# Kernel tuning notes

Measured on AMD Instinct MI355X. Metric: run time of the kernel, lower is better.

The kernel has to match this reference:

```python
import jax, jax.numpy as jnp
import numpy as np

ALPHA = 0.0  # module init alpha
BETA = 1.0   # default beta in set_target_with_data


def setup_inputs() -> dict:
    key = jax.random.key(0)
    k1, k2, k3, k4 = jax.random.split(key, 4)
    B, H, KP, N, D = 4, 16, 512, 4096, 64
    return {
        "K": jax.random.normal(k1, (B, H, KP, D), dtype=jnp.float32),
        "V": jax.random.normal(k2, (B, H, KP, D), dtype=jnp.float32),
        "xk": jax.random.normal(k3, (B, H, N, D), dtype=jnp.float32),
        "xv": jax.random.normal(k4, (B, H, N, D), dtype=jnp.float32),
    }


def reference(K, V, xk, xv):
    # set_target_with_data with dist_metric='dot', beta=1.0, beta2=None
    # dists: (B, H, k, n) = K @ xk^T
    dists = jnp.einsum('bhkd,bhnd->bhkn', K, xk)
    # softmax over the memory-slot axis (dim=-2)
    dk = jax.nn.softmax(BETA * dists, axis=-2)
    # normalize over the data axis (dim=-1)
    dkx = dk / jnp.sum(dk, axis=-1, keepdims=True)
    # weighted readout of data queries/values
    K_target = jnp.einsum('bhkn,bhnd->bhkd', dkx, xk)
    V_target = jnp.einsum('bhkn,bhnd->bhkd', dkx, xv)
    # set_target: grads used by maximize-SGD update
    gK = (1.0 - ALPHA) * (K_target - K)
    gV = (1.0 - ALPHA) * (V_target - V)
    return jnp.stack((gK, gV), axis=0)  # (2, B, H, k, d)
```

## Files before the change

kernel.cpp:

```cpp
#include <hip/hip_runtime.h>
#include <hip/hip_bf16.h>

typedef __bf16 bf16_t;
typedef __attribute__((ext_vector_type(8))) __bf16 bf16x8;
typedef __attribute__((ext_vector_type(4))) float f32x4;
typedef __attribute__((ext_vector_type(16))) float f32x16;

#define BH 64
#define KP 512
#define NN 4096
#define DD 64
#define GSZ (BH * KP * DD)

#define MFMA16(a, b, c) __builtin_amdgcn_mfma_f32_16x16x32_bf16((a), (b), (c), 0, 0, 0)
#define MFMA32(a, b, c) __builtin_amdgcn_mfma_f32_32x32x16_bf16((a), (b), (c), 0, 0, 0)

__device__ __forceinline__ bf16x8 cvt8v(const f32x4 lo, const f32x4 hi) {
  bf16x8 r;
  r[0] = (bf16_t)lo[0]; r[1] = (bf16_t)lo[1]; r[2] = (bf16_t)lo[2]; r[3] = (bf16_t)lo[3];
  r[4] = (bf16_t)hi[0]; r[5] = (bf16_t)hi[1]; r[6] = (bf16_t)hi[2]; r[7] = (bf16_t)hi[3];
  return r;
}
__device__ __forceinline__ bf16x8 cvt8(const float* __restrict__ p) {
  return cvt8v(*(const f32x4*)p, *(const f32x4*)(p + 4));
}
__device__ __forceinline__ unsigned pack2(float a, float b) {
  union { bf16_t h[2]; unsigned u; } x;
  x.h[0] = (bf16_t)a; x.h[1] = (bf16_t)b;
  return x.u;
}

__device__ __forceinline__ void stage16(bf16_t* lds_base, const bf16_t* gsrc) {
  __builtin_amdgcn_global_load_lds(
      (const __attribute__((address_space(1))) void*)gsrc,
      (__attribute__((address_space(3))) void*)lds_base, 16, 0, 0);
}

__global__ __launch_bounds__(256) void hop_prep(
    const float* __restrict__ xk, const float* __restrict__ xv,
    bf16_t* __restrict__ xk16, bf16_t* __restrict__ xkT16, bf16_t* __restrict__ xvT16)
{
  __shared__ __align__(16) bf16_t T[64 * 72];
  const int t = threadIdx.x;
  const int n0 = blockIdx.x * 64;
  const int bh = blockIdx.y;
  const int row = t >> 2;
  const int d0  = (t & 3) * 16;
  const int dcol = t >> 2;
  const int nb   = (t & 3) * 16;
  const size_t gb  = (size_t)bh * NN * DD;
  const size_t gbT = (size_t)bh * DD * NN;

  {
    const float* src = xk + gb + (size_t)(n0 + row) * DD + d0;
    const f32x4 a0 = *(const f32x4*)(src);
    const f32x4 a1 = *(const f32x4*)(src + 4);
    const f32x4 a2 = *(const f32x4*)(src + 8);
    const f32x4 a3 = *(const f32x4*)(src + 12);
    const bf16x8 lo = cvt8v(a0, a1), hi = cvt8v(a2, a3);
    bf16_t* dn = xk16 + gb + (size_t)(n0 + row) * DD + d0;
    *(bf16x8*)(dn)     = lo;
    *(bf16x8*)(dn + 8) = hi;
    *(bf16x8*)(T + row * 72 + d0)     = lo;
    *(bf16x8*)(T + row * 72 + d0 + 8) = hi;
  }
  __syncthreads();
  {
    bf16x8 o0, o1;
    #pragma unroll
    for (int j = 0; j < 8; j++) o0[j] = T[(nb + j) * 72 + dcol];
    #pragma unroll
    for (int j = 0; j < 8; j++) o1[j] = T[(nb + 8 + j) * 72 + dcol];
    bf16_t* dT = xkT16 + gbT + (size_t)dcol * NN + n0 + nb;
    *(bf16x8*)(dT)     = o0;
    *(bf16x8*)(dT + 8) = o1;
  }
  __syncthreads();
  {
    const float* src = xv + gb + (size_t)(n0 + row) * DD + d0;
    const f32x4 a0 = *(const f32x4*)(src);
    const f32x4 a1 = *(const f32x4*)(src + 4);
    const f32x4 a2 = *(const f32x4*)(src + 8);
    const f32x4 a3 = *(const f32x4*)(src + 12);
    *(bf16x8*)(T + row * 72 + d0)     = cvt8v(a0, a1);
    *(bf16x8*)(T + row * 72 + d0 + 8) = cvt8v(a2, a3);
  }
  __syncthreads();
  {
    bf16x8 o0, o1;
    #pragma unroll
    for (int j = 0; j < 8; j++) o0[j] = T[(nb + j) * 72 + dcol];
    #pragma unroll
    for (int j = 0; j < 8; j++) o1[j] = T[(nb + 8 + j) * 72 + dcol];
    bf16_t* dT = xvT16 + gbT + (size_t)dcol * NN + n0 + nb;
    *(bf16x8*)(dT)     = o0;
    *(bf16x8*)(dT + 8) = o1;
  }
}

__global__ __launch_bounds__(256) void hop_pass1(
    const float* __restrict__ Km, const bf16_t* __restrict__ xk16,
    float* __restrict__ inv_colsum)
{
  __shared__ __align__(16) bf16_t Ks[128 * 72];

  const int tid  = threadIdx.x;
  const int wave = tid >> 6, lane = tid & 63;
  const int col  = lane & 15, quad = lane >> 4;
  const int bid  = blockIdx.x;
  const int bh   = (bid & 7) + 8 * ((bid >> 3) & 7);
  const int n0   = (bid >> 6) * 256 + wave * 64;

  const float*  Kb   = Km   + (size_t)bh * KP * DD;
  const bf16_t* xkb  = xk16 + (size_t)bh * NN * DD;

  bf16x8 bf[4][2];
  #pragma unroll
  for (int nsub = 0; nsub < 4; nsub++) {
    const bf16_t* p = xkb + (size_t)(n0 + nsub * 16 + col) * DD + quad * 8;
    bf[nsub][0] = *(const bf16x8*)(p);
    bf[nsub][1] = *(const bf16x8*)(p + 32);
  }

  float colacc[4] = {0.f, 0.f, 0.f, 0.f};
  const int srow = tid >> 1, sdo = (tid & 1) * 32;

  for (int kc = 0; kc < KP; kc += 128) {
    __syncthreads();
    const float* src = Kb + (size_t)(kc + srow) * DD + sdo;
    #pragma unroll
    for (int u = 0; u < 4; u++) {
      const f32x4 p0 = *(const f32x4*)(src + 8 * u);
      const f32x4 p1 = *(const f32x4*)(src + 8 * u + 4);
      *(bf16x8*)(Ks + srow * 72 + sdo + 8 * u) = cvt8v(p0, p1);
    }
    __syncthreads();
    #pragma unroll
    for (int ks = 0; ks < 8; ks++) {
      const bf16x8 a0 = *(const bf16x8*)(Ks + (ks * 16 + col) * 72 + quad * 8);
      const bf16x8 a1 = *(const bf16x8*)(Ks + (ks * 16 + col) * 72 + 32 + quad * 8);
      #pragma unroll
      for (int nsub = 0; nsub < 4; nsub++) {
        f32x4 c = {0.f, 0.f, 0.f, 0.f};
        c = MFMA16(a0, bf[nsub][0], c);
        c = MFMA16(a1, bf[nsub][1], c);
        colacc[nsub] += __expf(c[0]) + __expf(c[1]) + __expf(c[2]) + __expf(c[3]);
      }
    }
  }
  #pragma unroll
  for (int nsub = 0; nsub < 4; nsub++) {
    colacc[nsub] += __shfl_xor(colacc[nsub], 16, 64);
    colacc[nsub] += __shfl_xor(colacc[nsub], 32, 64);
  }
  float v = colacc[0];
  v = (quad == 1) ? colacc[1] : v;
  v = (quad == 2) ? colacc[2] : v;
  v = (quad == 3) ? colacc[3] : v;
  inv_colsum[bh * NN + n0 + quad * 16 + col] = 1.0f / v;
}

#define NT 64

__global__ __launch_bounds__(256) void hop_pass2(
    const float* __restrict__ Km, const float* __restrict__ Vm,
    const bf16_t* __restrict__ xk16, const bf16_t* __restrict__ xkT16,
    const bf16_t* __restrict__ xvT16,
    const float* __restrict__ inv_colsum, float* __restrict__ out)
{
  __shared__ __align__(16) bf16_t xks[2][NT * DD];
  __shared__ __align__(16) bf16_t xkT[2][DD * NT];
  __shared__ __align__(16) bf16_t xvT[2][DD * NT];
  __shared__ float rows_lds[4][32];

  const int tid  = threadIdx.x;
  const int wave = tid >> 6, lane = tid & 63;
  const int col  = lane & 31, hi = lane >> 5;
  const int bid  = blockIdx.x;
  const int m    = bid >> 3;
  const int bh   = (bid & 7) + 8 * (m >> 2);
  const int kblk = m & 3;
  const int k0w  = kblk * 128 + wave * 32;

  const float*  Kb   = Km    + (size_t)bh * KP * DD;
  const float*  Vb   = Vm    + (size_t)bh * KP * DD;
  const bf16_t* xkb  = xk16  + (size_t)bh * NN * DD;
  const bf16_t* xkTb = xkT16 + (size_t)bh * DD * NN;
  const bf16_t* xvTb = xvT16 + (size_t)bh * DD * NN;
  const float*  inv  = inv_colsum + bh * NN;

  bf16x8 bk[4];
  #pragma unroll
  for (int t = 0; t < 4; t++)
    bk[t] = cvt8(Kb + (size_t)(k0w + col) * DD + t * 16 + hi * 8);

  f32x16 accK[2], accV[2];
  #pragma unroll
  for (int i = 0; i < 2; i++) {
    #pragma unroll
    for (int r = 0; r < 16; r++) { accK[i][r] = 0.f; accV[i][r] = 0.f; }
  }
  float rowacc = 0.f;

  const int srl = lane >> 3;
  const int r0  = wave * 16 + srl;
  const int r1  = r0 + 8;
  const int sb  = ((lane & 7) ^ srl) * 8;
  const int lb0 = (wave * 2 + 0) * 512;
  const int lb1 = (wave * 2 + 1) * 512;

  stage16(&xks[0][lb0], xkb + (size_t)r0 * DD + sb);
  stage16(&xks[0][lb1], xkb + (size_t)r1 * DD + sb);
  stage16(&xkT[0][lb0], xkTb + (size_t)r0 * NN + sb);
  stage16(&xkT[0][lb1], xkTb + (size_t)r1 * NN + sb);
  stage16(&xvT[0][lb0], xvTb + (size_t)r0 * NN + sb);
  stage16(&xvT[0][lb1], xvTb + (size_t)r1 * NN + sb);
  __syncthreads();

  int cur = 0;
  for (int n0 = 0; n0 < NN; n0 += NT) {
    if (n0 + NT < NN) {
      const int nx = n0 + NT;
      const int nb2 = cur ^ 1;
      stage16(&xks[nb2][lb0], xkb + (size_t)(nx + r0) * DD + sb);
      stage16(&xks[nb2][lb1], xkb + (size_t)(nx + r1) * DD + sb);
      stage16(&xkT[nb2][lb0], xkTb + (size_t)r0 * NN + nx + sb);
      stage16(&xkT[nb2][lb1], xkTb + (size_t)r1 * NN + nx + sb);
      stage16(&xvT[nb2][lb0], xvTb + (size_t)r0 * NN + nx + sb);
      stage16(&xvT[nb2][lb1], xvTb + (size_t)r1 * NN + nx + sb);
    }

    const bf16_t* xs = xks[cur];
    bf16x8 wa[4];

    #pragma unroll
    for (int nh = 0; nh < 2; nh++) {
      f32x4 icv[4];
      #pragma unroll
      for (int q = 0; q < 4; q++)
        icv[q] = *(const f32x4*)(inv + n0 + 32 * nh + 8 * q + 4 * hi);

      const int n  = nh * 32 + col;
      const int rb = n * DD;
      f32x16 s;
      #pragma unroll
      for (int r = 0; r < 16; r++) s[r] = 0.f;
      #pragma unroll
      for (int t = 0; t < 4; t++) {
        const bf16x8 a = *(const bf16x8*)(xs + rb + (((2 * t + hi) ^ (n & 7)) << 3));
        s = MFMA32(a, bk[t], s);
      }
      #pragma unroll
      for (int b = 0; b < 2; b++) {
        float p[8];
        #pragma unroll
        for (int j = 0; j < 8; j++)
          p[j] = __expf(s[8 * b + j]) * icv[2 * b + (j >> 2)][j & 3];
        rowacc += ((p[0] + p[1]) + (p[2] + p[3])) + ((p[4] + p[5]) + (p[6] + p[7]));
        unsigned q0a = pack2(p[0], p[1]), q0b = pack2(p[2], p[3]);
        unsigned q1a = pack2(p[4], p[5]), q1b = pack2(p[6], p[7]);
        asm("v_permlane32_swap_b32 %0, %1" : "+v"(q0a), "+v"(q1a));
        asm("v_permlane32_swap_b32 %0, %1" : "+v"(q0b), "+v"(q1b));
        union { unsigned u[4]; bf16x8 v; } f;
        f.u[0] = q0a; f.u[1] = q0b; f.u[2] = q1a; f.u[3] = q1b;
        wa[nh * 2 + b] = f.v;
      }
    }

    #pragma unroll
    for (int dg = 0; dg < 2; dg++) {
      const int d   = dg * 32 + col;
      const int rbd = d * NT;
      const bf16_t* kp = xkT[cur];
      const bf16_t* vp = xvT[cur];
      #pragma unroll
      for (int c = 0; c < 4; c++) {
        const int off = rbd + (((2 * c + hi) ^ (d & 7)) << 3);
        const bf16x8 bkf = *(const bf16x8*)(kp + off);
        const bf16x8 bvf = *(const bf16x8*)(vp + off);
        accK[dg] = MFMA32(wa[c], bkf, accK[dg]);
        accV[dg] = MFMA32(wa[c], bvf, accV[dg]);
      }
    }

    __syncthreads();
    cur ^= 1;
  }

  rowacc += __shfl_xor(rowacc, 32, 64);
  rows_lds[wave][col] = 1.0f / rowacc;

  const size_t base = (size_t)bh * KP * DD;
  #pragma unroll
  for (int dg = 0; dg < 2; dg++) {
    #pragma unroll
    for (int r = 0; r < 16; r++) {
      const int kw = (r & 3) + 8 * (r >> 2) + 4 * hi;
      const float invr = rows_lds[wave][kw];
      const int k = k0w + kw;
      const int d = dg * 32 + col;
      const size_t idx = base + (size_t)k * DD + d;
      out[idx]       = accK[dg][r] * invr - Kb[(size_t)k * DD + d];
      out[GSZ + idx] = accV[dg][r] * invr - Vb[(size_t)k * DD + d];
    }
  }
}

#define PW 72

__global__ __launch_bounds__(256) void hop_pass1_fb(
    const float* __restrict__ Km, const float* __restrict__ xk,
    float* __restrict__ inv_colsum)
{
  __shared__ __align__(16) bf16_t Ks[128 * 72];
  const int tid  = threadIdx.x;
  const int wave = tid >> 6, lane = tid & 63;
  const int col  = lane & 15, quad = lane >> 4;
  const int bh = blockIdx.y;
  const int n0 = blockIdx.x * 256 + wave * 64;
  const float* Kb  = Km + (size_t)bh * KP * DD;
  const float* xkb = xk + (size_t)bh * NN * DD;
  bf16x8 bf[4][2];
  #pragma unroll
  for (int nsub = 0; nsub < 4; nsub++) {
    const float* p = xkb + (size_t)(n0 + nsub * 16 + col) * DD + quad * 8;
    bf[nsub][0] = cvt8(p);
    bf[nsub][1] = cvt8(p + 32);
  }
  float colacc[4] = {0.f, 0.f, 0.f, 0.f};
  const int srow = tid >> 1, sdo = (tid & 1) * 32;
  for (int kc = 0; kc < KP; kc += 128) {
    __syncthreads();
    const float* src = Kb + (size_t)(kc + srow) * DD + sdo;
    #pragma unroll
    for (int u = 0; u < 4; u++) {
      const f32x4 p0 = *(const f32x4*)(src + 8 * u);
      const f32x4 p1 = *(const f32x4*)(src + 8 * u + 4);
      *(bf16x8*)(Ks + srow * 72 + sdo + 8 * u) = cvt8v(p0, p1);
    }
    __syncthreads();
    #pragma unroll
    for (int ks = 0; ks < 8; ks++) {
      const bf16x8 a0 = *(const bf16x8*)(Ks + (ks * 16 + col) * 72 + quad * 8);
      const bf16x8 a1 = *(const bf16x8*)(Ks + (ks * 16 + col) * 72 + 32 + quad * 8);
      #pragma unroll
      for (int nsub = 0; nsub < 4; nsub++) {
        f32x4 c = {0.f, 0.f, 0.f, 0.f};
        c = MFMA16(a0, bf[nsub][0], c);
        c = MFMA16(a1, bf[nsub][1], c);
        colacc[nsub] += __expf(c[0]) + __expf(c[1]) + __expf(c[2]) + __expf(c[3]);
      }
    }
  }
  #pragma unroll
  for (int nsub = 0; nsub < 4; nsub++) {
    colacc[nsub] += __shfl_xor(colacc[nsub], 16, 64);
    colacc[nsub] += __shfl_xor(colacc[nsub], 32, 64);
  }
  float v = colacc[0];
  v = (quad == 1) ? colacc[1] : v;
  v = (quad == 2) ? colacc[2] : v;
  v = (quad == 3) ? colacc[3] : v;
  inv_colsum[bh * NN + n0 + quad * 16 + col] = 1.0f / v;
}

__global__ __launch_bounds__(256) void hop_pass2_fb(
    const float* __restrict__ Km, const float* __restrict__ Vm,
    const float* __restrict__ xk, const float* __restrict__ xv,
    const float* __restrict__ inv_colsum, float* __restrict__ out)
{
  __shared__ __align__(16) bf16_t xksf[NT * PW];
  __shared__ __align__(16) bf16_t xkTf[DD * NT];
  __shared__ __align__(16) bf16_t xvTf[DD * NT];
  __shared__ __align__(16) bf16_t wtf[4][16 * PW];

  const int tid  = threadIdx.x;
  const int wave = tid >> 6, lane = tid & 63;
  const int col  = lane & 15, quad = lane >> 4;
  const int bh   = blockIdx.x >> 3;
  const int k0   = (blockIdx.x & 7) * 64 + wave * 16;

  const float* Kb  = Km + (size_t)bh * KP * DD;
  const float* Vb  = Vm + (size_t)bh * KP * DD;
  const float* xkb = xk + (size_t)bh * NN * DD;
  const float* xvb = xv + (size_t)bh * NN * DD;
  const float* inv = inv_colsum + bh * NN;

  const bf16x8 ak0 = cvt8(Kb + (size_t)(k0 + col) * DD + quad * 8);
  const bf16x8 ak1 = cvt8(Kb + (size_t)(k0 + col) * DD + 32 + quad * 8);

  f32x4 accK[4], accV[4];
  #pragma unroll
  for (int i = 0; i < 4; i++) {
    accK[i] = (f32x4){0.f, 0.f, 0.f, 0.f};
    accV[i] = (f32x4){0.f, 0.f, 0.f, 0.f};
  }
  float rows_part = 0.f;

  const int sn = tid >> 2;
  const int sd = (tid & 3) * 16;
  const int shi = sn >> 3, slo = sn & 7;

  for (int n0 = 0; n0 < NN; n0 += NT) {
    f32x4 gk[4], gv[4];
    #pragma unroll
    for (int u = 0; u < 4; u++) {
      gk[u] = *(const f32x4*)(xkb + (size_t)(n0 + sn) * DD + sd + 4 * u);
      gv[u] = *(const f32x4*)(xvb + (size_t)(n0 + sn) * DD + sd + 4 * u);
    }
    float ic[4];
    #pragma unroll
    for (int nsub = 0; nsub < 4; nsub++) ic[nsub] = inv[n0 + nsub * 16 + col];

    __syncthreads();
    *(bf16x8*)(xksf + sn * PW + sd)     = cvt8v(gk[0], gk[1]);
    *(bf16x8*)(xksf + sn * PW + sd + 8) = cvt8v(gk[2], gk[3]);
    #pragma unroll
    for (int j = 0; j < 16; j++) {
      const int d   = sd + j;
      const int off = d * NT + (((shi) ^ (d >> 3)) << 3) + slo;
      xkTf[off] = (bf16_t)gk[j >> 2][j & 3];
      xvTf[off] = (bf16_t)gv[j >> 2][j & 3];
    }
    __syncthreads();

    f32x4 s[4];
    #pragma unroll
    for (int nsub = 0; nsub < 4; nsub++) {
      const bf16x8 b0 = *(const bf16x8*)(xksf + (nsub * 16 + col) * PW + quad * 8);
      const bf16x8 b1 = *(const bf16x8*)(xksf + (nsub * 16 + col) * PW + 32 + quad * 8);
      f32x4 c = {0.f, 0.f, 0.f, 0.f};
      c = MFMA16(ak0, b0, c);
      c = MFMA16(ak1, b1, c);
      s[nsub] = c;
    }
    bf16_t* wr = wtf[wave];
    #pragma unroll
    for (int nsub = 0; nsub < 4; nsub++) {
      #pragma unroll
      for (int r = 0; r < 4; r++)
        wr[(quad * 4 + r) * PW + nsub * 16 + col] = (bf16_t)(__expf(s[nsub][r]) * ic[nsub]);
    }
    const bf16x8 wa0 = *(const bf16x8*)(wr + col * PW + quad * 8);
    const bf16x8 wa1 = *(const bf16x8*)(wr + col * PW + 32 + quad * 8);
    #pragma unroll
    for (int j = 0; j < 8; j++) rows_part += (float)wa0[j] + (float)wa1[j];

    #pragma unroll
    for (int dt = 0; dt < 4; dt++) {
      const int d = dt * 16 + col, dhi = d >> 3;
      const bf16x8 bk0 = *(const bf16x8*)(xkTf + d * NT + ((quad ^ dhi) << 3));
      const bf16x8 bk1 = *(const bf16x8*)(xkTf + d * NT + (((4 + quad) ^ dhi) << 3));
      const bf16x8 bv0 = *(const bf16x8*)(xvTf + d * NT + ((quad ^ dhi) << 3));
      const bf16x8 bv1 = *(const bf16x8*)(xvTf + d * NT + (((4 + quad) ^ dhi) << 3));
      accK[dt] = MFMA16(wa0, bk0, accK[dt]);
      accK[dt] = MFMA16(wa1, bk1, accK[dt]);
      accV[dt] = MFMA16(wa0, bv0, accV[dt]);
      accV[dt] = MFMA16(wa1, bv1, accV[dt]);
    }
  }

  float rs = rows_part;
  rs += __shfl_xor(rs, 16, 64);
  rs += __shfl_xor(rs, 32, 64);
  float invrs[4];
  #pragma unroll
  for (int r = 0; r < 4; r++) invrs[r] = 1.0f / __shfl(rs, quad * 4 + r, 64);

  const size_t base = (size_t)bh * KP * DD;
  #pragma unroll
  for (int dt = 0; dt < 4; dt++) {
    #pragma unroll
    for (int r = 0; r < 4; r++) {
      const int k = k0 + quad * 4 + r;
      const int d = dt * 16 + col;
      const size_t idx = base + (size_t)k * DD + d;
      out[idx]       = accK[dt][r] * invrs[r] - Kb[(size_t)k * DD + d];
      out[GSZ + idx] = accV[dt][r] * invrs[r] - Vb[(size_t)k * DD + d];
    }
  }
}

extern "C" void kernel_launch(void* const* d_in, const int* in_sizes, int n_in,
                              void* d_out, int out_size, void* d_ws, size_t ws_size,
                              hipStream_t stream)
{
  (void)in_sizes; (void)n_in; (void)out_size;
  const float* Km = (const float*)d_in[0];
  const float* Vm = (const float*)d_in[1];
  const float* xk = (const float*)d_in[2];
  const float* xv = (const float*)d_in[3];
  float* out = (float*)d_out;
  float* inv_colsum = (float*)d_ws;

  const size_t SCRE = (size_t)BH * NN * DD;
  const size_t NEED = (size_t)BH * NN * sizeof(float) + 3 * SCRE * sizeof(bf16_t);

  if (ws_size >= NEED) {
    bf16_t* xk16  = (bf16_t*)((char*)d_ws + (size_t)BH * NN * sizeof(float));
    bf16_t* xkT16 = xk16 + SCRE;
    bf16_t* xvT16 = xkT16 + SCRE;
    hop_prep<<<dim3(NN / 64, BH), 256, 0, stream>>>(xk, xv, xk16, xkT16, xvT16);
    hop_pass1<<<dim3((NN / 256) * BH), 256, 0, stream>>>(Km, xk16, inv_colsum);
    hop_pass2<<<dim3(BH * 4), 256, 0, stream>>>(Km, Vm, xk16, xkT16, xvT16,
                                                inv_colsum, out);
  } else {
    hop_pass1_fb<<<dim3(NN / 256, BH), 256, 0, stream>>>(Km, xk, inv_colsum);
    hop_pass2_fb<<<dim3(BH * (KP / 64)), 256, 0, stream>>>(Km, Vm, xk, xv,
                                                           inv_colsum, out);
  }
}
```

Before: 329.7 us.

## Split pass2 over the data axis into two halves with a reduction kernel

Splits the second pass along the N (data) dimension into two halves, so twice as many blocks (512 instead of 256) can fill the GPU. Each half writes partial K/V accumulators and partial row sums to workspace, and a new elementwise kernel combines them, normalises and subtracts K/V. A second fallback path with a 16x16 MFMA variant of pass2 is also added for a smaller workspace. The cost is an extra kernel launch plus extra global traffic for the partial results, and the path depends on the workspace being large enough.

```diff
diff --git a/kernel.cpp b/kernel.cpp
--- a/kernel.cpp
+++ b/kernel.cpp
@@ -11,6 +11,8 @@
 #define NN 4096
 #define DD 64
 #define GSZ (BH * KP * DD)
+#define NT 64
+#define NHALF 2048
 
 #define MFMA16(a, b, c) __builtin_amdgcn_mfma_f32_16x16x32_bf16((a), (b), (c), 0, 0, 0)
 #define MFMA32(a, b, c) __builtin_amdgcn_mfma_f32_32x32x16_bf16((a), (b), (c), 0, 0, 0)
@@ -160,30 +162,29 @@
   inv_colsum[bh * NN + n0 + quad * 16 + col] = 1.0f / v;
 }
 
-#define NT 64
-
-__global__ __launch_bounds__(256) void hop_pass2(
-    const float* __restrict__ Km, const float* __restrict__ Vm,
+__global__ __launch_bounds__(256) void hop_pass2s(
+    const float* __restrict__ Km,
     const bf16_t* __restrict__ xk16, const bf16_t* __restrict__ xkT16,
     const bf16_t* __restrict__ xvT16,
-    const float* __restrict__ inv_colsum, float* __restrict__ out)
+    const float* __restrict__ inv_colsum,
+    float* __restrict__ pK, float* __restrict__ pV, float* __restrict__ prs)
 {
   __shared__ __align__(16) bf16_t xks[2][NT * DD];
   __shared__ __align__(16) bf16_t xkT[2][DD * NT];
   __shared__ __align__(16) bf16_t xvT[2][DD * NT];
-  __shared__ float rows_lds[4][32];
 
   const int tid  = threadIdx.x;
   const int wave = tid >> 6, lane = tid & 63;
   const int col  = lane & 31, hi = lane >> 5;
   const int bid  = blockIdx.x;
-  const int m    = bid >> 3;
-  const int bh   = (bid & 7) + 8 * (m >> 2);
-  const int kblk = m & 3;
+  const int bh   = (bid & 7) + 8 * ((bid >> 3) & 7);
+  const int sub  = bid >> 6;
+  const int kblk = sub & 3;
+  const int nh   = sub >> 2;
   const int k0w  = kblk * 128 + wave * 32;
+  const int nbase = nh * NHALF;
 
   const float*  Kb   = Km    + (size_t)bh * KP * DD;
-  const float*  Vb   = Vm    + (size_t)bh * KP * DD;
   const bf16_t* xkb  = xk16  + (size_t)bh * NN * DD;
   const bf16_t* xkTb = xkT16 + (size_t)bh * DD * NN;
   const bf16_t* xvTb = xvT16 + (size_t)bh * DD * NN;
@@ -209,17 +210,17 @@
   const int lb0 = (wave * 2 + 0) * 512;
   const int lb1 = (wave * 2 + 1) * 512;
 
-  stage16(&xks[0][lb0], xkb + (size_t)r0 * DD + sb);
-  stage16(&xks[0][lb1], xkb + (size_t)r1 * DD + sb);
-  stage16(&xkT[0][lb0], xkTb + (size_t)r0 * NN + sb);
-  stage16(&xkT[0][lb1], xkTb + (size_t)r1 * NN + sb);
-  stage16(&xvT[0][lb0], xvTb + (size_t)r0 * NN + sb);
-  stage16(&xvT[0][lb1], xvTb + (size_t)r1 * NN + sb);
+  stage16(&xks[0][lb0], xkb + (size_t)(nbase + r0) * DD + sb);
+  stage16(&xks[0][lb1], xkb + (size_t)(nbase + r1) * DD + sb);
+  stage16(&xkT[0][lb0], xkTb + (size_t)r0 * NN + nbase + sb);
+  stage16(&xkT[0][lb1], xkTb + (size_t)r1 * NN + nbase + sb);
+  stage16(&xvT[0][lb0], xvTb + (size_t)r0 * NN + nbase + sb);
+  stage16(&xvT[0][lb1], xvTb + (size_t)r1 * NN + nbase + sb);
   __syncthreads();
 
   int cur = 0;
-  for (int n0 = 0; n0 < NN; n0 += NT) {
-    if (n0 + NT < NN) {
+  for (int n0 = nbase; n0 < nbase + NHALF; n0 += NT) {
+    if (n0 + NT < nbase + NHALF) {
       const int nx = n0 + NT;
       const int nb2 = cur ^ 1;
       stage16(&xks[nb2][lb0], xkb + (size_t)(nx + r0) * DD + sb);
@@ -234,13 +235,13 @@
     bf16x8 wa[4];
 
     #pragma unroll
-    for (int nh = 0; nh < 2; nh++) {
+    for (int g = 0; g < 2; g++) {
       f32x4 icv[4];
       #pragma unroll
       for (int q = 0; q < 4; q++)
-        icv[q] = *(const f32x4*)(inv + n0 + 32 * nh + 8 * q + 4 * hi);
-
-      const int n  = nh * 32 + col;
+        icv[q] = *(const f32x4*)(inv + n0 + 32 * g + 8 * q + 4 * hi);
+
+      const int n  = g * 32 + col;
       const int rb = n * DD;
       f32x16 s;
       #pragma unroll
@@ -263,7 +264,7 @@
         asm("v_permlane32_swap_b32 %0, %1" : "+v"(q0b), "+v"(q1b));
         union { unsigned u[4]; bf16x8 v; } f;
         f.u[0] = q0a; f.u[1] = q0b; f.u[2] = q1a; f.u[3] = q1b;
-        wa[nh * 2 + b] = f.v;
+        wa[g * 2 + b] = f.v;
       }
     }
 
@@ -288,20 +289,189 @@
   }
 
   rowacc += __shfl_xor(rowacc, 32, 64);
-  rows_lds[wave][col] = 1.0f / rowacc;
-
-  const size_t base = (size_t)bh * KP * DD;
+  if (hi == 0) prs[((size_t)nh * BH + bh) * KP + k0w + col] = rowacc;
+
+  float* pKb = pK + ((size_t)(nh * BH + bh) * KP) * DD;
+  float* pVb = pV + ((size_t)(nh * BH + bh) * KP) * DD;
   #pragma unroll
   for (int dg = 0; dg < 2; dg++) {
     #pragma unroll
     for (int r = 0; r < 16; r++) {
       const int kw = (r & 3) + 8 * (r >> 2) + 4 * hi;
-      const float invr = rows_lds[wave][kw];
       const int k = k0w + kw;
       const int d = dg * 32 + col;
+      pKb[(size_t)k * DD + d] = accK[dg][r];
+      pVb[(size_t)k * DD + d] = accV[dg][r];
+    }
+  }
+}
+
+__global__ __launch_bounds__(256) void hop_fin(
+    const float* __restrict__ Km, const float* __restrict__ Vm,
+    const float* __restrict__ pK, const float* __restrict__ pV,
+    const float* __restrict__ prs, float* __restrict__ out)
+{
+  const int t = blockIdx.x * 256 + threadIdx.x;
+  const size_t e  = (size_t)t * 8;
+  const size_t kk = e >> 6;
+  const size_t off = e;
+  const size_t plane = (size_t)BH * KP * DD;
+
+  const float invr = 1.0f / (prs[kk] + prs[(size_t)BH * KP + kk]);
+
+  const f32x4 ka0 = *(const f32x4*)(pK + off);
+  const f32x4 ka1 = *(const f32x4*)(pK + off + 4);
+  const f32x4 kb0 = *(const f32x4*)(pK + plane + off);
+  const f32x4 kb1 = *(const f32x4*)(pK + plane + off + 4);
+  const f32x4 va0 = *(const f32x4*)(pV + off);
+  const f32x4 va1 = *(const f32x4*)(pV + off + 4);
+  const f32x4 vb0 = *(const f32x4*)(pV + plane + off);
+  const f32x4 vb1 = *(const f32x4*)(pV + plane + off + 4);
+  const f32x4 K0  = *(const f32x4*)(Km + off);
+  const f32x4 K1  = *(const f32x4*)(Km + off + 4);
+  const f32x4 V0  = *(const f32x4*)(Vm + off);
+  const f32x4 V1  = *(const f32x4*)(Vm + off + 4);
+
+  f32x4 rk0 = (ka0 + kb0) * invr - K0;
+  f32x4 rk1 = (ka1 + kb1) * invr - K1;
+  f32x4 rv0 = (va0 + vb0) * invr - V0;
+  f32x4 rv1 = (va1 + vb1) * invr - V1;
+
+  *(f32x4*)(out + off)            = rk0;
+  *(f32x4*)(out + off + 4)        = rk1;
+  *(f32x4*)(out + GSZ + off)      = rv0;
+  *(f32x4*)(out + GSZ + off + 4)  = rv1;
+}
+
+__global__ __launch_bounds__(256) void hop_pass2m(
+    const float* __restrict__ Km, const float* __restrict__ Vm,
+    const bf16_t* __restrict__ xk16, const bf16_t* __restrict__ xkT16,
+    const bf16_t* __restrict__ xvT16,
+    const float* __restrict__ inv_colsum, float* __restrict__ out)
+{
+  __shared__ __align__(16) bf16_t xks[2][NT * DD];
+  __shared__ __align__(16) bf16_t xkT[2][DD * NT];
+  __shared__ __align__(16) bf16_t xvT[2][DD * NT];
+  __shared__ __align__(16) bf16_t wt[4][16 * 72];
+
+  const int tid  = threadIdx.x;
+  const int wave = tid >> 6, lane = tid & 63;
+  const int col  = lane & 15, quad = lane >> 4;
+  const int bid  = blockIdx.x;
+  const int bh   = (bid & 7) + 8 * ((bid >> 3) & 7);
+  const int k0   = (bid >> 6) * 64 + wave * 16;
+
+  const float*  Kb   = Km    + (size_t)bh * KP * DD;
+  const float*  Vb   = Vm    + (size_t)bh * KP * DD;
+  const bf16_t* xkb  = xk16  + (size_t)bh * NN * DD;
+  const bf16_t* xkTb = xkT16 + (size_t)bh * DD * NN;
+  const bf16_t* xvTb = xvT16 + (size_t)bh * DD * NN;
+  const float*  inv  = inv_colsum + bh * NN;
+
+  const bf16x8 ak0 = cvt8(Kb + (size_t)(k0 + col) * DD + quad * 8);
+  const bf16x8 ak1 = cvt8(Kb + (size_t)(k0 + col) * DD + 32 + quad * 8);
+
+  f32x4 accK[4], accV[4];
+  #pragma unroll
+  for (int i = 0; i < 4; i++) {
+    accK[i] = (f32x4){0.f, 0.f, 0.f, 0.f};
+    accV[i] = (f32x4){0.f, 0.f, 0.f, 0.f};
+  }
+  float rows_part = 0.f;
+
+  const int srl = lane >> 3;
+  const int r0  = wave * 16 + srl;
+  const int r1  = r0 + 8;
+  const int sb  = ((lane & 7) ^ srl) * 8;
+  const int lb0 = (wave * 2 + 0) * 512;
+  const int lb1 = (wave * 2 + 1) * 512;
+
+  stage16(&xks[0][lb0], xkb + (size_t)r0 * DD + sb);
+  stage16(&xks[0][lb1], xkb + (size_t)r1 * DD + sb);
+  stage16(&xkT[0][lb0], xkTb + (size_t)r0 * NN + sb);
+  stage16(&xkT[0][lb1], xkTb + (size_t)r1 * NN + sb);
+  stage16(&xvT[0][lb0], xvTb + (size_t)r0 * NN + sb);
+  stage16(&xvT[0][lb1], xvTb + (size_t)r1 * NN + sb);
+  __syncthreads();
+
+  int cur = 0;
+  for (int n0 = 0; n0 < NN; n0 += NT) {
+    if (n0 + NT < NN) {
+      const int nx = n0 + NT;
+      const int nb2 = cur ^ 1;
+      stage16(&xks[nb2][lb0], xkb + (size_t)(nx + r0) * DD + sb);
+      stage16(&xks[nb2][lb1], xkb + (size_t)(nx + r1) * DD + sb);
+      stage16(&xkT[nb2][lb0], xkTb + (size_t)r0 * NN + nx + sb);
+      stage16(&xkT[nb2][lb1], xkTb + (size_t)r1 * NN + nx + sb);
+      stage16(&xvT[nb2][lb0], xvTb + (size_t)r0 * NN + nx + sb);
+      stage16(&xvT[nb2][lb1], xvTb + (size_t)r1 * NN + nx + sb);
+    }
+
+    float ic[4];
+    #pragma unroll
+    for (int ns = 0; ns < 4; ns++) ic[ns] = inv[n0 + ns * 16 + col];
+
+    const int key = col & 7;
+
+    f32x4 s[4];
+    #pragma unroll
+    for (int ns = 0; ns < 4; ns++) {
+      const bf16_t* bp = &xks[cur][(ns * 16 + col) * DD];
+      const bf16x8 b0 = *(const bf16x8*)(bp + 8 * (quad ^ key));
+      const bf16x8 b1 = *(const bf16x8*)(bp + 8 * ((quad + 4) ^ key));
+      f32x4 c = {0.f, 0.f, 0.f, 0.f};
+      c = MFMA16(ak0, b0, c);
+      c = MFMA16(ak1, b1, c);
+      s[ns] = c;
+    }
+    bf16_t* wr = wt[wave];
+    #pragma unroll
+    for (int ns = 0; ns < 4; ns++) {
+      #pragma unroll
+      for (int r = 0; r < 4; r++)
+        wr[(quad * 4 + r) * 72 + ns * 16 + col] = (bf16_t)(__expf(s[ns][r]) * ic[ns]);
+    }
+    const bf16x8 wa0 = *(const bf16x8*)(wr + col * 72 + quad * 8);
+    const bf16x8 wa1 = *(const bf16x8*)(wr + col * 72 + 32 + quad * 8);
+    #pragma unroll
+    for (int j = 0; j < 8; j++) rows_part += (float)wa0[j] + (float)wa1[j];
+
+    #pragma unroll
+    for (int dt = 0; dt < 4; dt++) {
+      const int d = dt * 16 + col;
+      const bf16_t* kp = &xkT[cur][d * NT];
+      const bf16_t* vp = &xvT[cur][d * NT];
+      const bf16x8 bk0 = *(const bf16x8*)(kp + 8 * (quad ^ key));
+      const bf16x8 bk1 = *(const bf16x8*)(kp + 8 * ((quad + 4) ^ key));
+      const bf16x8 bv0 = *(const bf16x8*)(vp + 8 * (quad ^ key));
+      const bf16x8 bv1 = *(const bf16x8*)(vp + 8 * ((quad + 4) ^ key));
+      accK[dt] = MFMA16(wa0, bk0, accK[dt]);
+      accK[dt] = MFMA16(wa1, bk1, accK[dt]);
+      accV[dt] = MFMA16(wa0, bv0, accV[dt]);
+      accV[dt] = MFMA16(wa1, bv1, accV[dt]);
+    }
+
+    __syncthreads();
+    cur ^= 1;
+  }
+
+  float rs = rows_part;
+  rs += __shfl_xor(rs, 16, 64);
+  rs += __shfl_xor(rs, 32, 64);
+  float invrs[4];
+  #pragma unroll
+  for (int r = 0; r < 4; r++) invrs[r] = 1.0f / __shfl(rs, quad * 4 + r, 64);
+
+  const size_t base = (size_t)bh * KP * DD;
+  #pragma unroll
+  for (int dt = 0; dt < 4; dt++) {
+    #pragma unroll
+    for (int r = 0; r < 4; r++) {
+      const int k = k0 + quad * 4 + r;
+      const int d = dt * 16 + col;
       const size_t idx = base + (size_t)k * DD + d;
-      out[idx]       = accK[dg][r] * invr - Kb[(size_t)k * DD + d];
-      out[GSZ + idx] = accV[dg][r] * invr - Vb[(size_t)k * DD + d];
+      out[idx]       = accK[dt][r] * invrs[r] - Kb[(size_t)k * DD + d];
+      out[GSZ + idx] = accV[dt][r] * invrs[r] - Vb[(size_t)k * DD + d];
     }
   }
 }
@@ -491,19 +661,36 @@
   const float* xk = (const float*)d_in[2];
   const float* xv = (const float*)d_in[3];
   float* out = (float*)d_out;
+
+  const size_t INVB = (size_t)BH * NN * sizeof(float);
+  const size_t SCRE = (size_t)BH * NN * DD;
+  const size_t NEED  = INVB + 3 * SCRE * sizeof(bf16_t);
+  const size_t PPART = (size_t)2 * BH * KP * DD;
+  const size_t NEED2 = NEED + (2 * PPART + (size_t)2 * BH * KP) * sizeof(float);
+
   float* inv_colsum = (float*)d_ws;
 
-  const size_t SCRE = (size_t)BH * NN * DD;
-  const size_t NEED = (size_t)BH * NN * sizeof(float) + 3 * SCRE * sizeof(bf16_t);
-
-  if (ws_size >= NEED) {
-    bf16_t* xk16  = (bf16_t*)((char*)d_ws + (size_t)BH * NN * sizeof(float));
+  if (ws_size >= NEED2) {
+    bf16_t* xk16  = (bf16_t*)((char*)d_ws + INVB);
+    bf16_t* xkT16 = xk16 + SCRE;
+    bf16_t* xvT16 = xkT16 + SCRE;
+    float*  pK    = (float*)(xvT16 + SCRE);
+    float*  pV    = pK + PPART;
+    float*  prs   = pV + PPART;
+    hop_prep<<<dim3(NN / 64, BH), 256, 0, stream>>>(xk, xv, xk16, xkT16, xvT16);
+    hop_pass1<<<dim3((NN / 256) * BH), 256, 0, stream>>>(Km, xk16, inv_colsum);
+    hop_pass2s<<<dim3(512), 256, 0, stream>>>(Km, xk16, xkT16, xvT16,
+                                              inv_colsum, pK, pV, prs);
+    hop_fin<<<dim3((BH * KP * DD) / (256 * 8)), 256, 0, stream>>>(Km, Vm, pK, pV,
+                                                                  prs, out);
+  } else if (ws_size >= NEED) {
+    bf16_t* xk16  = (bf16_t*)((char*)d_ws + INVB);
     bf16_t* xkT16 = xk16 + SCRE;
     bf16_t* xvT16 = xkT16 + SCRE;
     hop_prep<<<dim3(NN / 64, BH), 256, 0, stream>>>(xk, xv, xk16, xkT16, xvT16);
     hop_pass1<<<dim3((NN / 256) * BH), 256, 0, stream>>>(Km, xk16, inv_colsum);
-    hop_pass2<<<dim3(BH * 4), 256, 0, stream>>>(Km, Vm, xk16, xkT16, xvT16,
-                                                inv_colsum, out);
+    hop_pass2m<<<dim3(BH * (KP / 64)), 256, 0, stream>>>(Km, Vm, xk16, xkT16, xvT16,
+                                                         inv_colsum, out);
   } else {
     hop_pass1_fb<<<dim3(NN / 256, BH), 256, 0, stream>>>(Km, xk, inv_colsum);
     hop_pass2_fb<<<dim3(BH * (KP / 64)), 256, 0, stream>>>(Km, Vm, xk, xv,
```

New measurement: 303.3 us. 1.09x faster.

## Fuse prep into pass1 and split pass2 over N with reduction kernel

Applied to the files above, without the earlier changes.

Merges the bf16 conversion and transpose prep kernel into the column-sum pass, so each block converts its own xk/xv tiles and takes MFMA operands straight from LDS. Pass2 is split along the data axis into NS segments, raising the grid from 256 to 1024 blocks to fill more CUs. Per-segment partial K/V sums and row sums go to workspace, and a new finalize kernel reduces them, normalizes and subtracts K/V. This adds a kernel launch and extra partial-sum memory traffic in exchange for better occupancy of pass2.

```diff
diff --git a/kernel.cpp b/kernel.cpp
--- a/kernel.cpp
+++ b/kernel.cpp
@@ -11,6 +11,7 @@
 #define NN 4096
 #define DD 64
 #define GSZ (BH * KP * DD)
+#define NT 64
 
 #define MFMA16(a, b, c) __builtin_amdgcn_mfma_f32_16x16x32_bf16((a), (b), (c), 0, 0, 0)
 #define MFMA32(a, b, c) __builtin_amdgcn_mfma_f32_32x32x16_bf16((a), (b), (c), 0, 0, 0)
@@ -36,90 +37,89 @@
       (__attribute__((address_space(3))) void*)lds_base, 16, 0, 0);
 }
 
-__global__ __launch_bounds__(256) void hop_prep(
-    const float* __restrict__ xk, const float* __restrict__ xv,
-    bf16_t* __restrict__ xk16, bf16_t* __restrict__ xkT16, bf16_t* __restrict__ xvT16)
-{
-  __shared__ __align__(16) bf16_t T[64 * 72];
-  const int t = threadIdx.x;
-  const int n0 = blockIdx.x * 64;
-  const int bh = blockIdx.y;
-  const int row = t >> 2;
-  const int d0  = (t & 3) * 16;
-  const int dcol = t >> 2;
-  const int nb   = (t & 3) * 16;
-  const size_t gb  = (size_t)bh * NN * DD;
-  const size_t gbT = (size_t)bh * DD * NN;
-
-  {
-    const float* src = xk + gb + (size_t)(n0 + row) * DD + d0;
-    const f32x4 a0 = *(const f32x4*)(src);
-    const f32x4 a1 = *(const f32x4*)(src + 4);
-    const f32x4 a2 = *(const f32x4*)(src + 8);
-    const f32x4 a3 = *(const f32x4*)(src + 12);
-    const bf16x8 lo = cvt8v(a0, a1), hi = cvt8v(a2, a3);
-    bf16_t* dn = xk16 + gb + (size_t)(n0 + row) * DD + d0;
-    *(bf16x8*)(dn)     = lo;
-    *(bf16x8*)(dn + 8) = hi;
-    *(bf16x8*)(T + row * 72 + d0)     = lo;
-    *(bf16x8*)(T + row * 72 + d0 + 8) = hi;
-  }
-  __syncthreads();
-  {
-    bf16x8 o0, o1;
-    #pragma unroll
-    for (int j = 0; j < 8; j++) o0[j] = T[(nb + j) * 72 + dcol];
-    #pragma unroll
-    for (int j = 0; j < 8; j++) o1[j] = T[(nb + 8 + j) * 72 + dcol];
-    bf16_t* dT = xkT16 + gbT + (size_t)dcol * NN + n0 + nb;
-    *(bf16x8*)(dT)     = o0;
-    *(bf16x8*)(dT + 8) = o1;
-  }
-  __syncthreads();
-  {
-    const float* src = xv + gb + (size_t)(n0 + row) * DD + d0;
-    const f32x4 a0 = *(const f32x4*)(src);
-    const f32x4 a1 = *(const f32x4*)(src + 4);
-    const f32x4 a2 = *(const f32x4*)(src + 8);
-    const f32x4 a3 = *(const f32x4*)(src + 12);
-    *(bf16x8*)(T + row * 72 + d0)     = cvt8v(a0, a1);
-    *(bf16x8*)(T + row * 72 + d0 + 8) = cvt8v(a2, a3);
-  }
-  __syncthreads();
-  {
-    bf16x8 o0, o1;
-    #pragma unroll
-    for (int j = 0; j < 8; j++) o0[j] = T[(nb + j) * 72 + dcol];
-    #pragma unroll
-    for (int j = 0; j < 8; j++) o1[j] = T[(nb + 8 + j) * 72 + dcol];
-    bf16_t* dT = xvT16 + gbT + (size_t)dcol * NN + n0 + nb;
-    *(bf16x8*)(dT)     = o0;
-    *(bf16x8*)(dT + 8) = o1;
-  }
-}
-
-__global__ __launch_bounds__(256) void hop_pass1(
-    const float* __restrict__ Km, const bf16_t* __restrict__ xk16,
-    float* __restrict__ inv_colsum)
+__global__ __launch_bounds__(256) void hop_p1f(
+    const float* __restrict__ Km, const float* __restrict__ xk,
+    const float* __restrict__ xv,
+    bf16_t* __restrict__ xk16, bf16_t* __restrict__ xkT16,
+    bf16_t* __restrict__ xvT16, float* __restrict__ inv_colsum)
 {
   __shared__ __align__(16) bf16_t Ks[128 * 72];
+  bf16_t* T = Ks;
 
   const int tid  = threadIdx.x;
   const int wave = tid >> 6, lane = tid & 63;
   const int col  = lane & 15, quad = lane >> 4;
   const int bid  = blockIdx.x;
   const int bh   = (bid & 7) + 8 * ((bid >> 3) & 7);
-  const int n0   = (bid >> 6) * 256 + wave * 64;
-
-  const float*  Kb   = Km   + (size_t)bh * KP * DD;
-  const bf16_t* xkb  = xk16 + (size_t)bh * NN * DD;
+  const int nblk = (bid >> 6) * 256;
+
+  const float* Kb  = Km + (size_t)bh * KP * DD;
+  const size_t gb  = (size_t)bh * NN * DD;
+  const size_t gbT = (size_t)bh * DD * NN;
+
+  const int row  = tid >> 2;
+  const int d0   = (tid & 3) * 16;
+  const int dcol = tid >> 2;
+  const int nb   = (tid & 3) * 16;
 
   bf16x8 bf[4][2];
-  #pragma unroll
-  for (int nsub = 0; nsub < 4; nsub++) {
-    const bf16_t* p = xkb + (size_t)(n0 + nsub * 16 + col) * DD + quad * 8;
-    bf[nsub][0] = *(const bf16x8*)(p);
-    bf[nsub][1] = *(const bf16x8*)(p + 32);
+
+  #pragma unroll
+  for (int b = 0; b < 4; b++) {
+    const int nbase = nblk + b * 64;
+    {
+      const float* src = xk + gb + (size_t)(nbase + row) * DD + d0;
+      const f32x4 a0 = *(const f32x4*)(src);
+      const f32x4 a1 = *(const f32x4*)(src + 4);
+      const f32x4 a2 = *(const f32x4*)(src + 8);
+      const f32x4 a3 = *(const f32x4*)(src + 12);
+      const bf16x8 lo = cvt8v(a0, a1), hi = cvt8v(a2, a3);
+      bf16_t* dn = xk16 + gb + (size_t)(nbase + row) * DD + d0;
+      *(bf16x8*)(dn)     = lo;
+      *(bf16x8*)(dn + 8) = hi;
+      *(bf16x8*)(T + row * 72 + d0)     = lo;
+      *(bf16x8*)(T + row * 72 + d0 + 8) = hi;
+    }
+    __syncthreads();
+    {
+      bf16x8 o0, o1;
+      #pragma unroll
+      for (int j = 0; j < 8; j++) o0[j] = T[(nb + j) * 72 + dcol];
+      #pragma unroll
+      for (int j = 0; j < 8; j++) o1[j] = T[(nb + 8 + j) * 72 + dcol];
+      bf16_t* dT = xkT16 + gbT + (size_t)dcol * NN + nbase + nb;
+      *(bf16x8*)(dT)     = o0;
+      *(bf16x8*)(dT + 8) = o1;
+      if (wave == b) {
+        #pragma unroll
+        for (int nsub = 0; nsub < 4; nsub++) {
+          bf[nsub][0] = *(const bf16x8*)(T + (nsub * 16 + col) * 72 + quad * 8);
+          bf[nsub][1] = *(const bf16x8*)(T + (nsub * 16 + col) * 72 + 32 + quad * 8);
+        }
+      }
+    }
+    __syncthreads();
+    {
+      const float* src = xv + gb + (size_t)(nbase + row) * DD + d0;
+      const f32x4 a0 = *(const f32x4*)(src);
+      const f32x4 a1 = *(const f32x4*)(src + 4);
+      const f32x4 a2 = *(const f32x4*)(src + 8);
+      const f32x4 a3 = *(const f32x4*)(src + 12);
+      *(bf16x8*)(T + row * 72 + d0)     = cvt8v(a0, a1);
+      *(bf16x8*)(T + row * 72 + d0 + 8) = cvt8v(a2, a3);
+    }
+    __syncthreads();
+    {
+      bf16x8 o0, o1;
+      #pragma unroll
+      for (int j = 0; j < 8; j++) o0[j] = T[(nb + j) * 72 + dcol];
+      #pragma unroll
+      for (int j = 0; j < 8; j++) o1[j] = T[(nb + 8 + j) * 72 + dcol];
+      bf16_t* dT = xvT16 + gbT + (size_t)dcol * NN + nbase + nb;
+      *(bf16x8*)(dT)     = o0;
+      *(bf16x8*)(dT + 8) = o1;
+    }
+    __syncthreads();
   }
 
   float colacc[4] = {0.f, 0.f, 0.f, 0.f};
@@ -157,33 +157,35 @@
   v = (quad == 1) ? colacc[1] : v;
   v = (quad == 2) ? colacc[2] : v;
   v = (quad == 3) ? colacc[3] : v;
-  inv_colsum[bh * NN + n0 + quad * 16 + col] = 1.0f / v;
-}
-
-#define NT 64
-
-__global__ __launch_bounds__(256) void hop_pass2(
-    const float* __restrict__ Km, const float* __restrict__ Vm,
+  inv_colsum[bh * NN + nblk + wave * 64 + quad * 16 + col] = 1.0f / v;
+}
+
+template <int NS>
+__global__ __launch_bounds__(256) void hop_pass2s(
+    const float* __restrict__ Km,
     const bf16_t* __restrict__ xk16, const bf16_t* __restrict__ xkT16,
     const bf16_t* __restrict__ xvT16,
-    const float* __restrict__ inv_colsum, float* __restrict__ out)
+    const float* __restrict__ inv_colsum,
+    float* __restrict__ pK, float* __restrict__ pV, float* __restrict__ prs)
 {
+  constexpr int NSEG = NN / NS;
+
   __shared__ __align__(16) bf16_t xks[2][NT * DD];
   __shared__ __align__(16) bf16_t xkT[2][DD * NT];
   __shared__ __align__(16) bf16_t xvT[2][DD * NT];
-  __shared__ float rows_lds[4][32];
 
   const int tid  = threadIdx.x;
   const int wave = tid >> 6, lane = tid & 63;
   const int col  = lane & 31, hi = lane >> 5;
   const int bid  = blockIdx.x;
-  const int m    = bid >> 3;
-  const int bh   = (bid & 7) + 8 * (m >> 2);
-  const int kblk = m & 3;
+  const int bh   = (bid & 7) + 8 * ((bid >> 3) & 7);
+  const int sub  = bid >> 6;
+  const int kblk = sub & 3;
+  const int nq   = sub >> 2;
   const int k0w  = kblk * 128 + wave * 32;
+  const int nbase = nq * NSEG;
 
   const float*  Kb   = Km    + (size_t)bh * KP * DD;
-  const float*  Vb   = Vm    + (size_t)bh * KP * DD;
   const bf16_t* xkb  = xk16  + (size_t)bh * NN * DD;
   const bf16_t* xkTb = xkT16 + (size_t)bh * DD * NN;
   const bf16_t* xvTb = xvT16 + (size_t)bh * DD * NN;
@@ -209,17 +211,17 @@
   const int lb0 = (wave * 2 + 0) * 512;
   const int lb1 = (wave * 2 + 1) * 512;
 
-  stage16(&xks[0][lb0], xkb + (size_t)r0 * DD + sb);
-  stage16(&xks[0][lb1], xkb + (size_t)r1 * DD + sb);
-  stage16(&xkT[0][lb0], xkTb + (size_t)r0 * NN + sb);
-  stage16(&xkT[0][lb1], xkTb + (size_t)r1 * NN + sb);
-  stage16(&xvT[0][lb0], xvTb + (size_t)r0 * NN + sb);
-  stage16(&xvT[0][lb1], xvTb + (size_t)r1 * NN + sb);
+  stage16(&xks[0][lb0], xkb + (size_t)(nbase + r0) * DD + sb);
+  stage16(&xks[0][lb1], xkb + (size_t)(nbase + r1) * DD + sb);
+  stage16(&xkT[0][lb0], xkTb + (size_t)r0 * NN + nbase + sb);
+  stage16(&xkT[0][lb1], xkTb + (size_t)r1 * NN + nbase + sb);
+  stage16(&xvT[0][lb0], xvTb + (size_t)r0 * NN + nbase + sb);
+  stage16(&xvT[0][lb1], xvTb + (size_t)r1 * NN + nbase + sb);
   __syncthreads();
 
   int cur = 0;
-  for (int n0 = 0; n0 < NN; n0 += NT) {
-    if (n0 + NT < NN) {
+  for (int n0 = nbase; n0 < nbase + NSEG; n0 += NT) {
+    if (n0 + NT < nbase + NSEG) {
       const int nx = n0 + NT;
       const int nb2 = cur ^ 1;
       stage16(&xks[nb2][lb0], xkb + (size_t)(nx + r0) * DD + sb);
@@ -234,13 +236,13 @@
     bf16x8 wa[4];
 
     #pragma unroll
-    for (int nh = 0; nh < 2; nh++) {
+    for (int g = 0; g < 2; g++) {
       f32x4 icv[4];
       #pragma unroll
       for (int q = 0; q < 4; q++)
-        icv[q] = *(const f32x4*)(inv + n0 + 32 * nh + 8 * q + 4 * hi);
-
-      const int n  = nh * 32 + col;
+        icv[q] = *(const f32x4*)(inv + n0 + 32 * g + 8 * q + 4 * hi);
+
+      const int n  = g * 32 + col;
       const int rb = n * DD;
       f32x16 s;
       #pragma unroll
@@ -263,7 +265,7 @@
         asm("v_permlane32_swap_b32 %0, %1" : "+v"(q0b), "+v"(q1b));
         union { unsigned u[4]; bf16x8 v; } f;
         f.u[0] = q0a; f.u[1] = q0b; f.u[2] = q1a; f.u[3] = q1b;
-        wa[nh * 2 + b] = f.v;
+        wa[g * 2 + b] = f.v;
       }
     }
 
@@ -288,22 +290,58 @@
   }
 
   rowacc += __shfl_xor(rowacc, 32, 64);
-  rows_lds[wave][col] = 1.0f / rowacc;
-
-  const size_t base = (size_t)bh * KP * DD;
+  if (hi == 0) prs[((size_t)nq * BH + bh) * KP + k0w + col] = rowacc;
+
+  float* pKb = pK + ((size_t)(nq * BH + bh) * KP) * DD;
+  float* pVb = pV + ((size_t)(nq * BH + bh) * KP) * DD;
   #pragma unroll
   for (int dg = 0; dg < 2; dg++) {
     #pragma unroll
     for (int r = 0; r < 16; r++) {
       const int kw = (r & 3) + 8 * (r >> 2) + 4 * hi;
-      const float invr = rows_lds[wave][kw];
       const int k = k0w + kw;
       const int d = dg * 32 + col;
-      const size_t idx = base + (size_t)k * DD + d;
-      out[idx]       = accK[dg][r] * invr - Kb[(size_t)k * DD + d];
-      out[GSZ + idx] = accV[dg][r] * invr - Vb[(size_t)k * DD + d];
-    }
-  }
+      pKb[(size_t)k * DD + d] = accK[dg][r];
+      pVb[(size_t)k * DD + d] = accV[dg][r];
+    }
+  }
+}
+
+template <int NS>
+__global__ __launch_bounds__(256) void hop_fin(
+    const float* __restrict__ Km, const float* __restrict__ Vm,
+    const float* __restrict__ pK, const float* __restrict__ pV,
+    const float* __restrict__ prs, float* __restrict__ out)
+{
+  const int t = blockIdx.x * 256 + threadIdx.x;
+  const size_t e   = (size_t)t * 8;
+  const size_t kk  = e >> 6;
+  const size_t off = e;
+  const size_t plane = (size_t)BH * KP * DD;
+
+  float rs = 0.f;
+  #pragma unroll
+  for (int s = 0; s < NS; s++) rs += prs[(size_t)s * BH * KP + kk];
+  const float invr = 1.0f / rs;
+
+  f32x4 sk0 = {0.f, 0.f, 0.f, 0.f}, sk1 = {0.f, 0.f, 0.f, 0.f};
+  f32x4 sv0 = {0.f, 0.f, 0.f, 0.f}, sv1 = {0.f, 0.f, 0.f, 0.f};
+  #pragma unroll
+  for (int s = 0; s < NS; s++) {
+    sk0 += *(const f32x4*)(pK + (size_t)s * plane + off);
+    sk1 += *(const f32x4*)(pK + (size_t)s * plane + off + 4);
+    sv0 += *(const f32x4*)(pV + (size_t)s * plane + off);
+    sv1 += *(const f32x4*)(pV + (size_t)s * plane + off + 4);
+  }
+  const f32x4 K0 = *(const f32x4*)(Km + off);
+  const f32x4 K1 = *(const f32x4*)(Km + off + 4);
+  const f32x4 V0 = *(const f32x4*)(Vm + off);
+  const f32x4 V1 = *(const f32x4*)(Vm + off + 4);
+
+  *(f32x4*)(out + off)           = sk0 * invr - K0;
+  *(f32x4*)(out + off + 4)       = sk1 * invr - K1;
+  *(f32x4*)(out + GSZ + off)     = sv0 * invr - V0;
+  *(f32x4*)(out + GSZ + off + 4) = sv1 * invr - V1;
 }
 
 #define PW 72
@@ -491,19 +529,39 @@
   const float* xk = (const float*)d_in[2];
   const float* xv = (const float*)d_in[3];
   float* out = (float*)d_out;
+
+  const size_t INVB  = (size_t)BH * NN * sizeof(float);
+  const size_t SCRE  = (size_t)BH * NN * DD;
+  const size_t BASE  = INVB + 3 * SCRE * sizeof(bf16_t);
+  const size_t PLANE = (size_t)BH * KP * DD;
+  const size_t NEED4 = BASE + (8 * PLANE + (size_t)4 * BH * KP) * sizeof(float);
+  const size_t NEED2 = BASE + (4 * PLANE + (size_t)2 * BH * KP) * sizeof(float);
+
   float* inv_colsum = (float*)d_ws;
 
-  const size_t SCRE = (size_t)BH * NN * DD;
-  const size_t NEED = (size_t)BH * NN * sizeof(float) + 3 * SCRE * sizeof(bf16_t);
-
-  if (ws_size >= NEED) {
-    bf16_t* xk16  = (bf16_t*)((char*)d_ws + (size_t)BH * NN * sizeof(float));
+  if (ws_size >= NEED2) {
+    bf16_t* xk16  = (bf16_t*)((char*)d_ws + INVB);
     bf16_t* xkT16 = xk16 + SCRE;
     bf16_t* xvT16 = xkT16 + SCRE;
-    hop_prep<<<dim3(NN / 64, BH), 256, 0, stream>>>(xk, xv, xk16, xkT16, xvT16);
-    hop_pass1<<<dim3((NN / 256) * BH), 256, 0, stream>>>(Km, xk16, inv_colsum);
-    hop_pass2<<<dim3(BH * 4), 256, 0, stream>>>(Km, Vm, xk16, xkT16, xvT16,
-                                                inv_colsum, out);
+    float*  pK    = (float*)(xvT16 + SCRE);
+
+    hop_p1f<<<dim3(1024), 256, 0, stream>>>(Km, xk, xv, xk16, xkT16, xvT16,
+                                            inv_colsum);
+    if (ws_size >= NEED4) {
+      float* pV  = pK + 4 * PLANE;
+      float* prs = pV + 4 * PLANE;
+      hop_pass2s<4><<<dim3(1024), 256, 0, stream>>>(Km, xk16, xkT16, xvT16,
+                                                    inv_colsum, pK, pV, prs);
+      hop_fin<4><<<dim3((BH * KP * DD) / (256 * 8)), 256, 0, stream>>>(
+          Km, Vm, pK, pV, prs, out);
+    } else {
+      float* pV  = pK + 2 * PLANE;
+      float* prs = pV + 2 * PLANE;
+      hop_pass2s<2><<<dim3(512), 256, 0, stream>>>(Km, xk16, xkT16, xvT16,
+                                                   inv_colsum, pK, pV, prs);
+      hop_fin<2><<<dim3((BH * KP * DD) / (256 * 8)), 256, 0, stream>>>(
+          Km, Vm, pK, pV, prs, out);
+    }
   } else {
     hop_pass1_fb<<<dim3(NN / 256, BH), 256, 0, stream>>>(Km, xk, inv_colsum);
     hop_pass2_fb<<<dim3(BH * (KP / 64)), 256, 0, stream>>>(Km, Vm, xk, xv,
```

Result: faster. 317.3 us (-3.8%).
